# Kernel optimization log

Measured on AMD Instinct MI355X. Metric: run time of the kernel, lower is better.

The kernel has to match this reference:

```python
import jax, jax.numpy as jnp
import numpy as np

BATCH, MAXPV = 32, 50
RULENUM, PROPNUM = 256, 256  # must be equal (eye(rulenum) * property_importance)
ENT_DIM, RULE_DIM = 128, 128
ENTITYNUM = 50000
THRESHOLD = 0.5


def _l2norm(x, eps=1e-12):
    # F.normalize(p=2, dim=-1)
    n = jnp.linalg.norm(x, axis=-1, keepdims=True)
    return x / jnp.clip(n, eps)


def setup_inputs() -> dict:
    key = jax.random.key(0)
    ks = jax.random.split(key, 20)
    d_in = ENT_DIM + RULE_DIM
    inp = {
        'property': jax.random.randint(ks[0], (BATCH, MAXPV), 0, ENTITYNUM),
        'value': jax.random.randint(ks[1], (BATCH, MAXPV), 0, ENTITYNUM),
        'samemask': jax.random.randint(ks[2], (BATCH, MAXPV), 0, 2),
        'padmask': jax.random.randint(ks[3], (BATCH, MAXPV), 0, 2),
        'rule_embedding': jax.random.normal(ks[4], (RULENUM, RULE_DIM), jnp.float32),
        'entity_table': jax.random.normal(ks[5], (ENTITYNUM, ENT_DIM), jnp.float32),
        # Linear weights stored (in, out); concat order in the original is (p_emb, rule_emb)
        'fc1_w': jax.random.normal(ks[6], (d_in, ENT_DIM), jnp.float32),
        'fc1_b': jax.random.normal(ks[7], (ENT_DIM,), jnp.float32) * 0.02,
        'fc2_w': jax.random.normal(ks[8], (d_in, ENT_DIM), jnp.float32),
        'fc2_b': jax.random.normal(ks[9], (ENT_DIM,), jnp.float32) * 0.02,
        'fc3_w': jax.random.normal(ks[10], (d_in, ENT_DIM), jnp.float32),
        'fc3_b': jax.random.normal(ks[11], (ENT_DIM,), jnp.float32) * 0.02,
        'fc4_w': jax.random.normal(ks[12], (ENT_DIM, 1), jnp.float32) * 0.05,
        'fc4_b': jax.random.normal(ks[13], (1,), jnp.float32) * 0.02,
        'fc5_w': jax.random.normal(ks[14], (ENT_DIM, 1), jnp.float32) * 0.05,
        'fc5_b': jax.random.normal(ks[15], (1,), jnp.float32) * 0.02,
        'fc6_w': jax.random.normal(ks[16], (ENT_DIM, ENT_DIM), jnp.float32) * 0.05,
        'fc6_b': jax.random.normal(ks[17], (ENT_DIM,), jnp.float32) * 0.02,
    }
    return inp


def reference(property, value, samemask, padmask, rule_embedding, entity_table,
              fc1_w, fc1_b, fc2_w, fc2_b, fc3_w, fc3_b,
              fc4_w, fc4_b, fc5_w, fc5_b, fc6_w, fc6_b):
    E = entity_table.shape[1]
    R = rule_embedding.shape[0]
    P = R  # propertynum == rulenum (required by eye() regularizer)

    p_emb = _l2norm(entity_table[property])   # (B, M, E)
    v_emb = _l2norm(entity_table[value])      # (B, M, E)
    r_emb = _l2norm(rule_embedding)           # (R, Dr)

    # cat(p, rule) -> Linear decomposed into two smaller matmuls (same math)
    def branch(w, b):
        return p_emb @ w[:E], r_emb @ w[E:] + b  # (B,M,Eo), (R,Eo)

    # s1 branch
    pa, ra = branch(fc1_w, fc1_b)
    h1 = jax.nn.relu(pa[:, None, :, :] + ra[None, :, None, :])   # (B,R,M,E)
    s1 = jax.nn.sigmoid(h1 @ fc4_w + fc4_b)[..., 0]              # (B,R,M)

    # p branch
    pb, rb = branch(fc2_w, fc2_b)
    h2 = jax.nn.relu(pb[:, None, :, :] + rb[None, :, None, :])
    p = jax.nn.sigmoid(h2 @ fc5_w + fc5_b)[..., 0]               # (B,R,M)

    # s2 branch
    pc, rc = branch(fc3_w, fc3_b)
    h3 = jax.nn.relu(pc[:, None, :, :] + rc[None, :, None, :])
    gv = _l2norm(h3 @ fc6_w + fc6_b)                             # (B,R,M,E)
    vb = v_emb[:, None, :, :]                                    # (B,1,M,E)
    denom = jnp.clip(jnp.linalg.norm(vb, axis=-1) * jnp.linalg.norm(gv, axis=-1), 1e-8)
    cos = jnp.sum(vb * gv, axis=-1) / denom
    s2 = 0.5 * cos + 0.5                                         # (B,R,M)

    score = p + (1.0 - p) * s2
    score = jnp.where(samemask[:, None, :] == 1, s1 * score, 1.0 - s1)

    # property importance K: fc1/fc4 on cat(prop_emb, rule_emb)
    prop_emb = _l2norm(entity_table[:P])                         # propertyids = arange(P)
    pi_h = jax.nn.relu((prop_emb @ fc1_w[:E])[None, :, :]
                       + (r_emb @ fc1_w[E:] + fc1_b)[:, None, :])  # (R,P,E)
    pi = jax.nn.sigmoid(pi_h @ fc4_w + fc4_b)[..., 0]            # (R,P)

    rule_mask = jnp.sum(pi * (pi > THRESHOLD), axis=-1) + 1.0    # (R,)

    score = score * padmask[:, None, :].astype(score.dtype)
    score = score * (s1 > THRESHOLD)
    score = jnp.sum(score, axis=-1) / rule_mask[None, :]          # (B,R)
    pooledscore = jnp.max(score, axis=1)                          # (B,)

    diag = jnp.eye(R, dtype=pi.dtype)
    reg = pi * diag + (1.0 - pi) * (1.0 - diag)
    reg = -jnp.log(reg + 1e-8) * (1.0 - diag + diag * R)
    reg_logits = jnp.mean(reg)
    return pooledscore, reg_logits
```

## Files before the change

kernel.cpp:

```cpp
#include <hip/hip_runtime.h>
#include <hip/hip_bf16.h>

#define BATCH 32
#define MAXPV 50
#define RN 256
#define PN 256
#define DIM 128
#define NPV (BATCH*MAXPV*DIM)
#define NI (BATCH*MAXPV)

typedef unsigned short u16;
typedef __attribute__((ext_vector_type(8))) short short8;
typedef __attribute__((ext_vector_type(4))) float f32x4;

__device__ float g_p[NPV], g_v[NPV], g_pa[NPV], g_pb[NPV], g_pc[NPV];
__device__ float g_pp1[PN*DIM], g_prop[PN*DIM], g_re[RN*DIM];
__device__ float g_raT[DIM*RN], g_rbT[DIM*RN];
__device__ float2 g_s1p[NI*RN];
__device__ float g_rmask[RN], g_regp[RN];
__device__ float g_scores[(size_t)NI*RN];
__device__ short8 g_bfrag[8][4][64];
__device__ float g_rcA[16*4*64*8];

__device__ __forceinline__ float bf2f(u16 u){ return __uint_as_float(((unsigned)u)<<16); }
__device__ __forceinline__ float LD(const void* p, size_t i, bool bf){
    return bf ? bf2f(((const u16*)p)[i]) : ((const float*)p)[i];
}
__device__ __forceinline__ int LDI(const void* p, size_t i, bool w64){
    return w64 ? (int)((const long long*)p)[i] : ((const int*)p)[i];
}
__device__ __forceinline__ short f2bf(float f){
    unsigned u = __float_as_uint(f);
    u = (u + 0x7FFFu + ((u>>16)&1u)) >> 16;
    return (short)u;
}
__device__ __forceinline__ unsigned f2bf2(float x, float y){
    float2 f; f.x=x; f.y=y;
    __hip_bfloat162 h = __float22bfloat162_rn(f);
    union { __hip_bfloat162 h; unsigned u; } c; c.h=h; return c.u;
}
__device__ __forceinline__ bool det_bf16(const void* ent){
    int l = threadIdx.x & 63;
    u16 v = ((const u16*)ent)[(size_t)2*(l*4)*977];
    int e = (v>>7)&0xFF;
    return __popcll(__ballot(e>=120 && e<=133)) >= 48;
}
__device__ __forceinline__ bool det_i64(const void* prop){
    int l = threadIdx.x & 63;
    bool z = (l<32) ? (((const unsigned*)prop)[2*l+1]==0u) : false;
    return __popcll(__ballot(z)) >= 30;
}
__device__ __forceinline__ float wred(float v){
#pragma unroll
    for(int o=32;o;o>>=1) v += __shfl_xor(v,o,64);
    return v;
}
__device__ __forceinline__ double wredd(double v){
#pragma unroll
    for(int o=32;o;o>>=1) v += __shfl_xor(v,o,64);
    return v;
}
__device__ __forceinline__ float wmax(float v){
#pragma unroll
    for(int o=32;o;o>>=1) v = fmaxf(v,__shfl_xor(v,o,64));
    return v;
}

__global__ void k_norm(const void* __restrict__ ent, const void* __restrict__ rule,
                       const void* __restrict__ prop, const void* __restrict__ val,
                       const void* __restrict__ fc6w){
    const bool bf = det_bf16(ent);
    const int blk = blockIdx.x, tid = threadIdx.x;
    if(blk >= 928){
        int nt = blk-928;
        int ks = tid>>6, lane = tid&63;
        int n = nt*16 + (lane&15);
        int k0 = ks*32 + (lane>>4)*8;
        short8 v;
#pragma unroll
        for(int j=0;j<8;j++) v[j] = f2bf(LD(fc6w,(size_t)(k0+j)*DIM + n, bf));
        g_bfrag[nt][ks][lane] = v;
        if(nt==0){ g_rmask[tid] = 1.f; g_regp[tid] = 0.f; }
        return;
    }
    const bool w64 = det_i64(prop);
    int row = blk*4 + (tid>>6);
    int l = tid & 63;
    const void* src; size_t off; float* dst;
    if(row < 1600){ src=ent; off=(size_t)LDI(prop,row,w64)*DIM; dst=g_p+(size_t)row*DIM; }
    else if(row < 3200){ int i=row-1600; src=ent; off=(size_t)LDI(val,i,w64)*DIM; dst=g_v+(size_t)i*DIM; }
    else if(row < 3456){ int i=row-3200; src=rule; off=(size_t)i*DIM; dst=g_re+(size_t)i*DIM; }
    else { int i=row-3456; src=ent; off=(size_t)i*DIM; dst=g_prop+(size_t)i*DIM; }
    float a = LD(src,off+l,bf), b = LD(src,off+l+64,bf);
    float n = fmaxf(sqrtf((float)wredd((double)a*a+(double)b*b)), 1e-12f);
    dst[l]=a/n; dst[l+64]=b/n;
}

__global__ __launch_bounds__(256) void k_mm(
    const void* __restrict__ ent,
    const void* __restrict__ fc1w, const void* __restrict__ fc2w, const void* __restrict__ fc3w,
    const void* __restrict__ fc1b, const void* __restrict__ fc2b, const void* __restrict__ fc3b){
    __shared__ float s_w[64*DIM];
    __shared__ float s_in[16*DIM];
    __shared__ float s_bias[DIM];
    const bool bf = det_bf16(ent);
    const int blk = blockIdx.x, tid = threadIdx.x;
    const float* in; const void* w; size_t woff=0; const void* bptr=nullptr;
    float* out=nullptr; int row0; int mode=0;
    if(blk < 100){ row0=blk*16; in=g_p; w=fc1w; out=g_pa; }
    else if(blk < 200){ row0=(blk-100)*16; in=g_p; w=fc2w; out=g_pb; }
    else if(blk < 300){ row0=(blk-200)*16; in=g_p; w=fc3w; out=g_pc; }
    else if(blk < 316){ row0=(blk-300)*16; in=g_re; w=fc1w; woff=DIM*DIM; bptr=fc1b; mode=1; }
    else if(blk < 332){ row0=(blk-316)*16; in=g_re; w=fc2w; woff=DIM*DIM; bptr=fc2b; mode=2; }
    else if(blk < 348){ row0=(blk-332)*16; in=g_re; w=fc3w; woff=DIM*DIM; bptr=fc3b; mode=3; }
    else { row0=(blk-348)*16; in=g_prop; w=fc1w; out=g_pp1; }
    for(int t=tid; t<16*DIM; t+=256) s_in[t] = in[(size_t)row0*DIM + t];
    if(tid<DIM) s_bias[tid] = bptr ? LD(bptr,tid,bf) : 0.f;
    const int j = tid & 127;
    const int rb8 = (tid>>7)*8;
    double acc[8] = {0,0,0,0,0,0,0,0};
    for(int half=0; half<2; half++){
        __syncthreads();
        for(int t=tid; t<64*DIM; t+=256)
            s_w[t] = LD(w, woff + (size_t)(half*64 + (t>>7))*DIM + (t&127), bf);
        __syncthreads();
        for(int k=0;k<64;k++){
            float wk = s_w[k*DIM + j];
#pragma unroll
            for(int rr=0;rr<8;rr++)
                acc[rr] += (double)s_in[(rb8+rr)*DIM + half*64 + k]*(double)wk;
        }
    }
    const double bj = (double)s_bias[j];
#pragma unroll
    for(int rr=0;rr<8;rr++){
        const int row = row0 + rb8 + rr;
        const float vv = (float)(bj + acc[rr]);
        if(mode==0)      out[(size_t)row*DIM + j] = vv;
        else if(mode==1) g_raT[j*256 + row] = vv;
        else if(mode==2) g_rbT[j*256 + row] = vv;
        else {
            int mt=row>>4, am=row&15, ks=j>>5, quad=(j>>3)&3, jj=j&7;
            g_rcA[((mt*4+ks)*64 + quad*16+am)*8 + jj] = vv;
        }
    }
}

__global__ __launch_bounds__(256) void k_gate(
    const void* __restrict__ ent,
    const void* __restrict__ fc4w, const void* __restrict__ fc4b,
    const void* __restrict__ fc5w, const void* __restrict__ fc5b){
    __shared__ float s_a[4][DIM], s_b[4][DIM], s_f5[DIM];
    __shared__ double s_f4[DIM];
    const bool bf = det_bf16(ent);
    const int blk = blockIdx.x, tid = threadIdx.x;
    const bool typeA = blk < 400;
    const int i0 = typeA ? blk*4 : (blk-400)*4;
    if(tid<DIM){ s_f4[tid]=(double)LD(fc4w,tid,bf); s_f5[tid]=LD(fc5w,tid,bf); }
    for(int t=tid; t<4*DIM; t+=256){
        int ii=t>>7, k=t&127;
        s_a[ii][k] = typeA ? g_pa[(size_t)(i0+ii)*DIM+k] : g_pp1[(size_t)(i0+ii)*DIM+k];
        if(typeA) s_b[ii][k] = g_pb[(size_t)(i0+ii)*DIM+k];
    }
    __syncthreads();
    const int r = tid;
    double d[4]={0.0,0.0,0.0,0.0}; float pq[4]={0.f,0.f,0.f,0.f};
    if(typeA){
        for(int k=0;k<DIM;k++){
            float rav = g_raT[k*256+r];
            float rbv = g_rbT[k*256+r];
            double f4k = s_f4[k]; float f5k = s_f5[k];
#pragma unroll
            for(int ii=0;ii<4;ii++){
                d[ii] += (double)fmaxf(s_a[ii][k]+rav,0.f)*f4k;
                pq[ii] = fmaf(fmaxf(s_b[ii][k]+rbv,0.f), f5k, pq[ii]);
            }
        }
    } else {
        for(int k=0;k<DIM;k++){
            float rav = g_raT[k*256+r];
            double f4k = s_f4[k];
#pragma unroll
            for(int ii=0;ii<4;ii++)
                d[ii] += (double)fmaxf(s_a[ii][k]+rav,0.f)*f4k;
        }
    }
    const double b4 = (double)LD(fc4b,0,bf);
    if(typeA){
        const float b5 = LD(fc5b,0,bf);
#pragma unroll
        for(int ii=0;ii<4;ii++){
            double sd = d[ii] + b4;
            float s1v = 1.f/(1.f+expf(-(float)sd));
            float p = 1.f/(1.f+expf(-(pq[ii] + b5)));
            float2 o; o.x = (sd > 0.0) ? s1v : -s1v; o.y = p;
            g_s1p[(size_t)(i0+ii)*RN + r] = o;
        }
    } else {
        float mask_sum = 0.f, reg_sum = 0.f;
#pragma unroll
        for(int ii=0;ii<4;ii++){
            int p = i0 + ii;
            double sd = d[ii] + b4;
            float piv = 1.f/(1.f+expf(-(float)sd));
            if(sd > 0.0) mask_sum += piv;
            float eff = (p==r) ? piv : (1.f - piv);
            float wgt = (p==r) ? (float)RN : 1.f;
            reg_sum += -logf(eff + 1e-8f)*wgt;
        }
        atomicAdd(&g_rmask[r], mask_sum);
        atomicAdd(&g_regp[r], reg_sum);
    }
}

__global__ __launch_bounds__(256) void k_main(
    const void* __restrict__ ent, const void* __restrict__ prop,
    const void* __restrict__ fc6b,
    const void* __restrict__ same, const void* __restrict__ pad){
    const int blk = blockIdx.x;
    const int i = blk >> 1, h = blk & 1;
    const bool w64 = det_i64(prop);
    if(LDI(same,i,w64)!=1 || LDI(pad,i,w64)!=1) return;
    const bool bf = det_bf16(ent);
    __shared__ float s_pc[DIM];
    __shared__ float s_st[128][4][2];
    const int tid = threadIdx.x, w = tid>>6, l = tid&63;
    const int am = l&15, quad = l>>4;

    if(tid < DIM) s_pc[tid] = g_pc[(size_t)i*DIM + tid];

    short8 bA[4], bB[4];
#pragma unroll
    for(int ks=0; ks<4; ks++){ bA[ks]=g_bfrag[2*w][ks][l]; bB[ks]=g_bfrag[2*w+1][ks][l]; }
    const int n0 = w*32 + am, n1 = n0 + 16;
    const float v0 = g_v[(size_t)i*DIM + n0], v1 = g_v[(size_t)i*DIM + n1];
    const float b60 = LD(fc6b, n0, bf), b61 = LD(fc6b, n1, bf);

    float vl = g_v[(size_t)i*DIM + l], vh = g_v[(size_t)i*DIM + l + 64];
    const float nvb = sqrtf(wred(vl*vl + vh*vh));
    __syncthreads();

    int mt = h*8;
    float4 c[8];
#pragma unroll
    for(int ks=0; ks<4; ks++){
        const float* rp = &g_rcA[((mt*4+ks)*64 + l)*8];
        c[2*ks]   = *(const float4*)rp;
        c[2*ks+1] = *(const float4*)(rp+4);
    }
    for(int mtl=0; mtl<8; mtl++){
        float4 n[8];
        if(mtl < 7){
#pragma unroll
            for(int ks=0; ks<4; ks++){
                const float* rp = &g_rcA[(((mt+1)*4+ks)*64 + l)*8];
                n[2*ks]   = *(const float4*)rp;
                n[2*ks+1] = *(const float4*)(rp+4);
            }
        }
        short8 a[4];
#pragma unroll
        for(int ks=0; ks<4; ks++){
            const float4 p0 = *(const float4*)&s_pc[ks*32 + quad*8];
            const float4 p1 = *(const float4*)&s_pc[ks*32 + quad*8 + 4];
            const float4 c0 = c[2*ks], c1 = c[2*ks+1];
            union { short8 s; unsigned u[4]; } t;
            t.u[0] = f2bf2(fmaxf(p0.x+c0.x,0.f), fmaxf(p0.y+c0.y,0.f));
            t.u[1] = f2bf2(fmaxf(p0.z+c0.z,0.f), fmaxf(p0.w+c0.w,0.f));
            t.u[2] = f2bf2(fmaxf(p1.x+c1.x,0.f), fmaxf(p1.y+c1.y,0.f));
            t.u[3] = f2bf2(fmaxf(p1.z+c1.z,0.f), fmaxf(p1.w+c1.w,0.f));
            a[ks] = t.s;
        }
        f32x4 acc0 = {0.f,0.f,0.f,0.f}, acc1 = {0.f,0.f,0.f,0.f};
#pragma unroll
        for(int ks=0; ks<4; ks++){
            acc0 = __builtin_amdgcn_mfma_f32_16x16x32_bf16(a[ks], bA[ks], acc0, 0,0,0);
            acc1 = __builtin_amdgcn_mfma_f32_16x16x32_bf16(a[ks], bB[ks], acc1, 0,0,0);
        }
#pragma unroll
        for(int q=0; q<4; q++){
            float x0 = acc0[q] + b60;
            float x1 = acc1[q] + b61;
            float ss = x0*x0 + x1*x1;
            float dv = x0*v0 + x1*v1;
#pragma unroll
            for(int o=1;o<16;o<<=1){ ss += __shfl_xor(ss,o,64); dv += __shfl_xor(dv,o,64); }
            if(am==0){
                int row = mtl*16 + quad*4 + q;
                s_st[row][w][0] = ss;
                s_st[row][w][1] = dv;
            }
        }
#pragma unroll
        for(int x=0;x<8;x++) c[x] = n[x];
        mt++;
    }
    __syncthreads();
    if(tid < 128){
        const int r = h*128 + tid;
        float ss = s_st[tid][0][0]+s_st[tid][1][0]+s_st[tid][2][0]+s_st[tid][3][0];
        float dv = s_st[tid][0][1]+s_st[tid][1][1]+s_st[tid][2][1]+s_st[tid][3][1];
        float2 sp = g_s1p[(size_t)i*RN + r];
        float s1 = fabsf(sp.x);
        float gate = (sp.x > 0.f) ? 1.f : 0.f;
        float pp = sp.y;
        float nx = sqrtf(ss);
        float clipnx = fmaxf(nx, 1e-12f);
        float gvn = nx/clipnx;
        float denom = fmaxf(nvb*gvn, 1e-8f);
        float cosv = (dv/clipnx)/denom;
        float s2 = 0.5f*cosv + 0.5f;
        float sc = s1*(pp + (1.f-pp)*s2);
        g_scores[(size_t)i*RN + r] = sc * gate;
    }
}

__global__ void k_fin(float* __restrict__ out, const void* __restrict__ prop,
                      const void* __restrict__ same, const void* __restrict__ pad){
    const bool w64 = det_i64(prop);
    const int blk = blockIdx.x, tid = threadIdx.x;
    const int w = tid>>6, l = tid&63;
    __shared__ float s[4];
    if(blk < 32){
        __shared__ int s_same[MAXPV], s_pad[MAXPV];
        if(tid < MAXPV){
            s_same[tid] = LDI(same, (size_t)blk*MAXPV + tid, w64);
            s_pad[tid]  = LDI(pad,  (size_t)blk*MAXPV + tid, w64);
        }
        __syncthreads();
        float ssum = 0.f;
        for(int pv=0; pv<MAXPV; pv++){
            if(!s_pad[pv]) continue;
            const size_t i = (size_t)blk*MAXPV + pv;
            if(s_same[pv]==1) ssum += g_scores[i*RN + tid];
            else { float sx = g_s1p[i*RN + tid].x; ssum += (sx > 0.f) ? (1.f - sx) : 0.f; }
        }
        float sc = ssum / g_rmask[tid];
        float m = wmax(sc);
        if(l==0) s[w]=m;
        __syncthreads();
        if(tid==0) out[blk] = fmaxf(fmaxf(s[0],s[1]), fmaxf(s[2],s[3]));
    } else {
        float v = g_regp[tid];
        v = wred(v);
        if(l==0) s[w]=v;
        __syncthreads();
        if(tid==0) out[32] = (s[0]+s[1]+s[2]+s[3]) / (float)(RN*PN);
    }
}

extern "C" void kernel_launch(void* const* d_in, const int* in_sizes, int n_in,
                              void* d_out, int out_size, void* d_ws, size_t ws_size,
                              hipStream_t stream){
    int map[18]; for(int i=0;i<18;i++) map[i]=i;
    if(n_in>=18 && in_sizes[0]==6400000){
        const int a[18] = {14,17,16,13,15,0,2,1,4,3,6,5,8,7,10,9,12,11};
        for(int i=0;i<18;i++) map[i]=a[i];
    }
    const void* prop = d_in[map[0]];
    const void* val  = d_in[map[1]];
    const void* same = d_in[map[2]];
    const void* pad  = d_in[map[3]];
    const void* rule = d_in[map[4]];
    const void* ent  = d_in[map[5]];
    const void* fc1w = d_in[map[6]];
    const void* fc1b = d_in[map[7]];
    const void* fc2w = d_in[map[8]];
    const void* fc2b = d_in[map[9]];
    const void* fc3w = d_in[map[10]];
    const void* fc3b = d_in[map[11]];
    const void* fc4w = d_in[map[12]];
    const void* fc4b = d_in[map[13]];
    const void* fc5w = d_in[map[14]];
    const void* fc5b = d_in[map[15]];
    const void* fc6w = d_in[map[16]];
    const void* fc6b = d_in[map[17]];

    k_norm<<<936, 256, 0, stream>>>(ent, rule, prop, val, fc6w);
    k_mm<<<364, 256, 0, stream>>>(ent, fc1w, fc2w, fc3w, fc1b, fc2b, fc3b);
    k_gate<<<464, 256, 0, stream>>>(ent, fc4w, fc4b, fc5w, fc5b);
    k_main<<<NI*2, 256, 0, stream>>>(ent, prop, fc6b, same, pad);
    k_fin<<<33, 256, 0, stream>>>((float*)d_out, prop, same, pad);
}
```

Before: 215.1 us.

## Fuse normalization into matmul and gating into main scoring kernel

Merges the L2-normalization kernel into the fc1/fc2/fc3 projection kernel so normalized rows go straight to shared memory, and merges the gate kernel into the main scoring kernel so s1/p are computed per item and kept in shared memory. This removes two launches and the global round-trips of g_p, g_v, g_re, g_prop and g_s1p. Gate computation now runs only for padded-in items, with non-same items writing their final score directly. In exchange, each scoring block recomputes the gate with only 128 active threads, and every projection block re-gathers and re-normalizes its input rows.

```diff
diff --git a/kernel.cpp b/kernel.cpp
--- a/kernel.cpp
+++ b/kernel.cpp
@@ -6,17 +6,15 @@
 #define RN 256
 #define PN 256
 #define DIM 128
-#define NPV (BATCH*MAXPV*DIM)
 #define NI (BATCH*MAXPV)
 
 typedef unsigned short u16;
 typedef __attribute__((ext_vector_type(8))) short short8;
 typedef __attribute__((ext_vector_type(4))) float f32x4;
 
-__device__ float g_p[NPV], g_v[NPV], g_pa[NPV], g_pb[NPV], g_pc[NPV];
-__device__ float g_pp1[PN*DIM], g_prop[PN*DIM], g_re[RN*DIM];
+__device__ float g_pa[NI*DIM], g_pb[NI*DIM], g_pc[NI*DIM];
+__device__ float g_pp1[PN*DIM];
 __device__ float g_raT[DIM*RN], g_rbT[DIM*RN];
-__device__ float2 g_s1p[NI*RN];
 __device__ float g_rmask[RN], g_regp[RN];
 __device__ float g_scores[(size_t)NI*RN];
 __device__ short8 g_bfrag[8][4][64];
@@ -66,13 +64,15 @@
     return v;
 }
 
-__global__ void k_norm(const void* __restrict__ ent, const void* __restrict__ rule,
-                       const void* __restrict__ prop, const void* __restrict__ val,
-                       const void* __restrict__ fc6w){
+__global__ __launch_bounds__(256) void k_pre(
+    const void* __restrict__ ent, const void* __restrict__ rule,
+    const void* __restrict__ prop, const void* __restrict__ fc6w,
+    const void* __restrict__ fc1w, const void* __restrict__ fc2w, const void* __restrict__ fc3w,
+    const void* __restrict__ fc1b, const void* __restrict__ fc2b, const void* __restrict__ fc3b){
     const bool bf = det_bf16(ent);
     const int blk = blockIdx.x, tid = threadIdx.x;
-    if(blk >= 928){
-        int nt = blk-928;
+    if(blk >= 364){
+        int nt = blk-364;
         int ks = tid>>6, lane = tid&63;
         int n = nt*16 + (lane&15);
         int k0 = ks*32 + (lane>>4)*8;
@@ -83,38 +83,36 @@
         if(nt==0){ g_rmask[tid] = 1.f; g_regp[tid] = 0.f; }
         return;
     }
-    const bool w64 = det_i64(prop);
-    int row = blk*4 + (tid>>6);
-    int l = tid & 63;
-    const void* src; size_t off; float* dst;
-    if(row < 1600){ src=ent; off=(size_t)LDI(prop,row,w64)*DIM; dst=g_p+(size_t)row*DIM; }
-    else if(row < 3200){ int i=row-1600; src=ent; off=(size_t)LDI(val,i,w64)*DIM; dst=g_v+(size_t)i*DIM; }
-    else if(row < 3456){ int i=row-3200; src=rule; off=(size_t)i*DIM; dst=g_re+(size_t)i*DIM; }
-    else { int i=row-3456; src=ent; off=(size_t)i*DIM; dst=g_prop+(size_t)i*DIM; }
-    float a = LD(src,off+l,bf), b = LD(src,off+l+64,bf);
-    float n = fmaxf(sqrtf((float)wredd((double)a*a+(double)b*b)), 1e-12f);
-    dst[l]=a/n; dst[l+64]=b/n;
-}
-
-__global__ __launch_bounds__(256) void k_mm(
-    const void* __restrict__ ent,
-    const void* __restrict__ fc1w, const void* __restrict__ fc2w, const void* __restrict__ fc3w,
-    const void* __restrict__ fc1b, const void* __restrict__ fc2b, const void* __restrict__ fc3b){
     __shared__ float s_w[64*DIM];
     __shared__ float s_in[16*DIM];
     __shared__ float s_bias[DIM];
-    const bool bf = det_bf16(ent);
-    const int blk = blockIdx.x, tid = threadIdx.x;
-    const float* in; const void* w; size_t woff=0; const void* bptr=nullptr;
-    float* out=nullptr; int row0; int mode=0;
-    if(blk < 100){ row0=blk*16; in=g_p; w=fc1w; out=g_pa; }
-    else if(blk < 200){ row0=(blk-100)*16; in=g_p; w=fc2w; out=g_pb; }
-    else if(blk < 300){ row0=(blk-200)*16; in=g_p; w=fc3w; out=g_pc; }
-    else if(blk < 316){ row0=(blk-300)*16; in=g_re; w=fc1w; woff=DIM*DIM; bptr=fc1b; mode=1; }
-    else if(blk < 332){ row0=(blk-316)*16; in=g_re; w=fc2w; woff=DIM*DIM; bptr=fc2b; mode=2; }
-    else if(blk < 348){ row0=(blk-332)*16; in=g_re; w=fc3w; woff=DIM*DIM; bptr=fc3b; mode=3; }
-    else { row0=(blk-348)*16; in=g_prop; w=fc1w; out=g_pp1; }
-    for(int t=tid; t<16*DIM; t+=256) s_in[t] = in[(size_t)row0*DIM + t];
+    const void* w; size_t woff=0; const void* bptr=nullptr;
+    float* out=nullptr; int row0; int mode=0; int srcsel;
+    if(blk < 300){
+        int wsel = blk/100; row0 = (blk%100)*16; srcsel = 0;
+        w   = (wsel==0)?fc1w:(wsel==1)?fc2w:fc3w;
+        out = (wsel==0)?g_pa:(wsel==1)?g_pb:g_pc;
+    } else if(blk < 348){
+        int rblk = blk-300; int wsel = rblk>>4; row0 = (rblk&15)*16; srcsel = 1;
+        w    = (wsel==0)?fc1w:(wsel==1)?fc2w:fc3w;
+        bptr = (wsel==0)?fc1b:(wsel==1)?fc2b:fc3b;
+        woff = DIM*DIM; mode = wsel+1;
+    } else { row0=(blk-348)*16; w=fc1w; out=g_pp1; srcsel=2; }
+    const bool w64 = (srcsel==0) ? det_i64(prop) : false;
+    {
+        const int l = tid & 63;
+        for(int it=0; it<4; it++){
+            int lr = it*4 + (tid>>6);
+            int row = row0 + lr;
+            const void* src; size_t off;
+            if(srcsel==0){ src=ent;  off=(size_t)LDI(prop,row,w64)*DIM; }
+            else if(srcsel==1){ src=rule; off=(size_t)row*DIM; }
+            else { src=ent; off=(size_t)row*DIM; }
+            float a = LD(src,off+l,bf), b = LD(src,off+l+64,bf);
+            float n = fmaxf(sqrtf((float)wredd((double)a*a+(double)b*b)), 1e-12f);
+            s_in[lr*DIM+l]=a/n; s_in[lr*DIM+l+64]=b/n;
+        }
+    }
     if(tid<DIM) s_bias[tid] = bptr ? LD(bptr,tid,bf) : 0.f;
     const int j = tid & 127;
     const int rb8 = (tid>>7)*8;
@@ -146,57 +144,34 @@
     }
 }
 
-__global__ __launch_bounds__(256) void k_gate(
-    const void* __restrict__ ent,
+__global__ __launch_bounds__(256) void k_score(
+    const void* __restrict__ ent, const void* __restrict__ prop, const void* __restrict__ val,
+    const void* __restrict__ same, const void* __restrict__ pad,
     const void* __restrict__ fc4w, const void* __restrict__ fc4b,
-    const void* __restrict__ fc5w, const void* __restrict__ fc5b){
-    __shared__ float s_a[4][DIM], s_b[4][DIM], s_f5[DIM];
-    __shared__ double s_f4[DIM];
+    const void* __restrict__ fc5w, const void* __restrict__ fc5b,
+    const void* __restrict__ fc6b){
+    const int blk = blockIdx.x, tid = threadIdx.x;
     const bool bf = det_bf16(ent);
-    const int blk = blockIdx.x, tid = threadIdx.x;
-    const bool typeA = blk < 400;
-    const int i0 = typeA ? blk*4 : (blk-400)*4;
-    if(tid<DIM){ s_f4[tid]=(double)LD(fc4w,tid,bf); s_f5[tid]=LD(fc5w,tid,bf); }
-    for(int t=tid; t<4*DIM; t+=256){
-        int ii=t>>7, k=t&127;
-        s_a[ii][k] = typeA ? g_pa[(size_t)(i0+ii)*DIM+k] : g_pp1[(size_t)(i0+ii)*DIM+k];
-        if(typeA) s_b[ii][k] = g_pb[(size_t)(i0+ii)*DIM+k];
-    }
-    __syncthreads();
-    const int r = tid;
-    double d[4]={0.0,0.0,0.0,0.0}; float pq[4]={0.f,0.f,0.f,0.f};
-    if(typeA){
+    if(blk >= NI*2){
+        __shared__ float s_a[4][DIM];
+        __shared__ double s_pf4[DIM];
+        const int i0 = (blk - NI*2)*4;
+        if(tid<DIM) s_pf4[tid]=(double)LD(fc4w,tid,bf);
+        for(int t=tid; t<4*DIM; t+=256){
+            int ii=t>>7, k=t&127;
+            s_a[ii][k] = g_pp1[(size_t)(i0+ii)*DIM+k];
+        }
+        __syncthreads();
+        const int r = tid;
+        double d[4]={0.0,0.0,0.0,0.0};
         for(int k=0;k<DIM;k++){
             float rav = g_raT[k*256+r];
-            float rbv = g_rbT[k*256+r];
-            double f4k = s_f4[k]; float f5k = s_f5[k];
-#pragma unroll
-            for(int ii=0;ii<4;ii++){
-                d[ii] += (double)fmaxf(s_a[ii][k]+rav,0.f)*f4k;
-                pq[ii] = fmaf(fmaxf(s_b[ii][k]+rbv,0.f), f5k, pq[ii]);
-            }
-        }
-    } else {
-        for(int k=0;k<DIM;k++){
-            float rav = g_raT[k*256+r];
-            double f4k = s_f4[k];
+            double f4k = s_pf4[k];
 #pragma unroll
             for(int ii=0;ii<4;ii++)
                 d[ii] += (double)fmaxf(s_a[ii][k]+rav,0.f)*f4k;
         }
-    }
-    const double b4 = (double)LD(fc4b,0,bf);
-    if(typeA){
-        const float b5 = LD(fc5b,0,bf);
-#pragma unroll
-        for(int ii=0;ii<4;ii++){
-            double sd = d[ii] + b4;
-            float s1v = 1.f/(1.f+expf(-(float)sd));
-            float p = 1.f/(1.f+expf(-(pq[ii] + b5)));
-            float2 o; o.x = (sd > 0.0) ? s1v : -s1v; o.y = p;
-            g_s1p[(size_t)(i0+ii)*RN + r] = o;
-        }
-    } else {
+        const double b4 = (double)LD(fc4b,0,bf);
         float mask_sum = 0.f, reg_sum = 0.f;
 #pragma unroll
         for(int ii=0;ii<4;ii++){
@@ -210,35 +185,75 @@
         }
         atomicAdd(&g_rmask[r], mask_sum);
         atomicAdd(&g_regp[r], reg_sum);
-    }
-}
-
-__global__ __launch_bounds__(256) void k_main(
-    const void* __restrict__ ent, const void* __restrict__ prop,
-    const void* __restrict__ fc6b,
-    const void* __restrict__ same, const void* __restrict__ pad){
-    const int blk = blockIdx.x;
+        return;
+    }
     const int i = blk >> 1, h = blk & 1;
     const bool w64 = det_i64(prop);
-    if(LDI(same,i,w64)!=1 || LDI(pad,i,w64)!=1) return;
-    const bool bf = det_bf16(ent);
-    __shared__ float s_pc[DIM];
+    if(LDI(pad,i,w64)!=1) return;
+    const bool issame = (LDI(same,i,w64)==1);
+
+    __shared__ float s_pa[DIM], s_pb[DIM], s_pc[DIM], s_v[DIM];
+    __shared__ float s_f5[DIM];
+    __shared__ double s_f4[DIM];
+    __shared__ float2 s_s1p[DIM];
     __shared__ float s_st[128][4][2];
-    const int tid = threadIdx.x, w = tid>>6, l = tid&63;
+
+    if(tid < DIM){
+        s_pa[tid] = g_pa[(size_t)i*DIM + tid];
+        s_pb[tid] = g_pb[(size_t)i*DIM + tid];
+        s_pc[tid] = g_pc[(size_t)i*DIM + tid];
+        s_f4[tid] = (double)LD(fc4w,tid,bf);
+        s_f5[tid] = LD(fc5w,tid,bf);
+    } else if(tid < 192){
+        const int l = tid - 128;
+        size_t off = (size_t)LDI(val,i,w64)*DIM;
+        float a = LD(ent,off+l,bf), b = LD(ent,off+l+64,bf);
+        float n = fmaxf(sqrtf((float)wredd((double)a*a+(double)b*b)), 1e-12f);
+        s_v[l]=a/n; s_v[l+64]=b/n;
+    }
+    __syncthreads();
+
+    if(tid < 128){
+        const int r = h*128 + tid;
+        double d = 0.0; float pq = 0.f;
+        if(issame){
+            for(int k=0;k<DIM;k++){
+                float rav = g_raT[k*256+r];
+                float rbv = g_rbT[k*256+r];
+                d += (double)fmaxf(s_pa[k]+rav,0.f)*s_f4[k];
+                pq = fmaf(fmaxf(s_pb[k]+rbv,0.f), s_f5[k], pq);
+            }
+        } else {
+            for(int k=0;k<DIM;k++){
+                float rav = g_raT[k*256+r];
+                d += (double)fmaxf(s_pa[k]+rav,0.f)*s_f4[k];
+            }
+        }
+        const double b4 = (double)LD(fc4b,0,bf);
+        double sd = d + b4;
+        float s1v = 1.f/(1.f+expf(-(float)sd));
+        if(issame){
+            const float b5 = LD(fc5b,0,bf);
+            float p = 1.f/(1.f+expf(-(pq + b5)));
+            float2 o; o.x = (sd > 0.0) ? s1v : -s1v; o.y = p;
+            s_s1p[tid] = o;
+        } else {
+            g_scores[(size_t)i*RN + r] = (sd > 0.0) ? (1.f - s1v) : 0.f;
+        }
+    }
+    if(!issame) return;
+    __syncthreads();
+
+    const int w = tid>>6, l = tid&63;
     const int am = l&15, quad = l>>4;
-
-    if(tid < DIM) s_pc[tid] = g_pc[(size_t)i*DIM + tid];
-
     short8 bA[4], bB[4];
 #pragma unroll
     for(int ks=0; ks<4; ks++){ bA[ks]=g_bfrag[2*w][ks][l]; bB[ks]=g_bfrag[2*w+1][ks][l]; }
     const int n0 = w*32 + am, n1 = n0 + 16;
-    const float v0 = g_v[(size_t)i*DIM + n0], v1 = g_v[(size_t)i*DIM + n1];
+    const float v0 = s_v[n0], v1 = s_v[n1];
     const float b60 = LD(fc6b, n0, bf), b61 = LD(fc6b, n1, bf);
-
-    float vl = g_v[(size_t)i*DIM + l], vh = g_v[(size_t)i*DIM + l + 64];
+    float vl = s_v[l], vh = s_v[l+64];
     const float nvb = sqrtf(wred(vl*vl + vh*vh));
-    __syncthreads();
 
     int mt = h*8;
     float4 c[8];
@@ -300,7 +315,7 @@
         const int r = h*128 + tid;
         float ss = s_st[tid][0][0]+s_st[tid][1][0]+s_st[tid][2][0]+s_st[tid][3][0];
         float dv = s_st[tid][0][1]+s_st[tid][1][1]+s_st[tid][2][1]+s_st[tid][3][1];
-        float2 sp = g_s1p[(size_t)i*RN + r];
+        float2 sp = s_s1p[tid];
         float s1 = fabsf(sp.x);
         float gate = (sp.x > 0.f) ? 1.f : 0.f;
         float pp = sp.y;
@@ -322,18 +337,13 @@
     const int w = tid>>6, l = tid&63;
     __shared__ float s[4];
     if(blk < 32){
-        __shared__ int s_same[MAXPV], s_pad[MAXPV];
-        if(tid < MAXPV){
-            s_same[tid] = LDI(same, (size_t)blk*MAXPV + tid, w64);
-            s_pad[tid]  = LDI(pad,  (size_t)blk*MAXPV + tid, w64);
-        }
+        __shared__ int s_pad[MAXPV];
+        if(tid < MAXPV) s_pad[tid] = LDI(pad, (size_t)blk*MAXPV + tid, w64);
         __syncthreads();
         float ssum = 0.f;
         for(int pv=0; pv<MAXPV; pv++){
             if(!s_pad[pv]) continue;
-            const size_t i = (size_t)blk*MAXPV + pv;
-            if(s_same[pv]==1) ssum += g_scores[i*RN + tid];
-            else { float sx = g_s1p[i*RN + tid].x; ssum += (sx > 0.f) ? (1.f - sx) : 0.f; }
+            ssum += g_scores[((size_t)blk*MAXPV + pv)*RN + tid];
         }
         float sc = ssum / g_rmask[tid];
         float m = wmax(sc);
@@ -376,9 +386,9 @@
     const void* fc6w = d_in[map[16]];
     const void* fc6b = d_in[map[17]];
 
-    k_norm<<<936, 256, 0, stream>>>(ent, rule, prop, val, fc6w);
-    k_mm<<<364, 256, 0, stream>>>(ent, fc1w, fc2w, fc3w, fc1b, fc2b, fc3b);
-    k_gate<<<464, 256, 0, stream>>>(ent, fc4w, fc4b, fc5w, fc5b);
-    k_main<<<NI*2, 256, 0, stream>>>(ent, prop, fc6b, same, pad);
+    k_pre<<<372, 256, 0, stream>>>(ent, rule, prop, fc6w,
+                                   fc1w, fc2w, fc3w, fc1b, fc2b, fc3b);
+    k_score<<<NI*2+64, 256, 0, stream>>>(ent, prop, val, same, pad,
+                                         fc4w, fc4b, fc5w, fc5b, fc6b);
     k_fin<<<33, 256, 0, stream>>>((float*)d_out, prop, same, pad);
 }
```

Measured after the change: 203.9 us. 1.05x faster.
